# Kernel optimization log

Measured on AMD Instinct MI355X. Metric: run time of the kernel, lower is better.

The kernel has to match this reference:

```python
import jax, jax.numpy as jnp
import numpy as np

PATCH = 5
PAD = PATCH // 2
EPS = 0.01
NP2 = PATCH * PATCH  # 25 elements per patch


def _conv(x, w, b):
    # VALID conv, NCHW / OIHW
    y = jax.lax.conv_general_dilated(x, w, (1, 1), 'VALID',
                                     dimension_numbers=('NCHW', 'OIHW', 'NCHW'))
    return y + b[None, :, None, None]


def _maxpool2(x):
    return jax.lax.reduce_window(x, -jnp.inf, jax.lax.max,
                                 (1, 1, 2, 2), (1, 1, 2, 2), 'VALID')


def _normed_patches(x):
    # x: [B,C,H,W] -> zero-mean unit-std 5x5 patches [B,C,H,W,25]
    B, C, H, W = x.shape
    xp = jnp.pad(x, ((0, 0), (0, 0), (PAD, PAD), (PAD, PAD)))
    p = jnp.stack([xp[:, :, u:u + H, v:v + W]
                   for u in range(PATCH) for v in range(PATCH)], axis=-1)
    mu = p.mean(axis=-1, keepdims=True)
    sd = p.std(axis=-1, keepdims=True)
    return (p - mu) / (sd + EPS)


def _normxcorr(X, Y):
    # patch-wise NCC: each 5x5 patch of X at (i,j) vs patches of Y at rows
    # i-2..i+2 (zero outside) and ALL W columns -> [B, C*5*W, H, W]
    B, C, H, W = X.shape
    Xn = _normed_patches(X)            # [B,C,H,W,25]
    Yn = _normed_patches(Y)            # [B,C,H,W,25]
    Ynp = jnp.pad(Yn, ((0, 0), (0, 0), (PAD, PAD), (0, 0), (0, 0)))
    # row-shifted views: d=0..4 corresponds to displacement d-2
    Ysh = jnp.stack([Ynp[:, :, d:d + H] for d in range(PATCH)], axis=2)  # [B,C,5,H,W,25]
    out = jnp.einsum('bcijp,bcdikp->bcdkij', Xn, Ysh) / NP2  # [B,C,5,W,H,W]
    return out.reshape(B, C * PATCH * W, H, W)  # C*5*12 = 1500 channels


def _branch(x, w1, b1, w2, b2):
    x = _maxpool2(jax.nn.relu(_conv(x, w1, b1)))
    x = _maxpool2(jax.nn.relu(_conv(x, w2, b2)))
    return x  # [B,25,37,12]


def setup_inputs() -> dict:
    key = jax.random.key(0)
    ks = jax.random.split(key, 10)
    B = 64

    def n(k, shp, s=0.05):
        return jax.random.normal(k, shp, dtype=jnp.float32) * s

    return {
        'x1': jax.random.normal(ks[0], (B, 3, 160, 60), dtype=jnp.float32),
        'x2': jax.random.normal(ks[1], (B, 3, 160, 60), dtype=jnp.float32),
        'w_conv1': n(ks[2], (20, 3, 5, 5)), 'b_conv1': jnp.zeros((20,), jnp.float32),
        'w_conv2': n(ks[3], (25, 20, 5, 5)), 'b_conv2': jnp.zeros((25,), jnp.float32),
        'w_red1': n(ks[4], (25, 1500, 1, 1)), 'b_red1': jnp.zeros((25,), jnp.float32),
        'w_red2': n(ks[5], (25, 25, 3, 3)), 'b_red2': jnp.zeros((25,), jnp.float32),
        'w_lin1': n(ks[6], (500, 25 * 17 * 5)), 'b_lin1': jnp.zeros((500,), jnp.float32),
        'w_lin2': n(ks[7], (2, 500)), 'b_lin2': jnp.zeros((2,), jnp.float32),
    }


def reference(x1, x2, w_conv1, b_conv1, w_conv2, b_conv2,
              w_red1, b_red1, w_red2, b_red2,
              w_lin1, b_lin1, w_lin2, b_lin2):
    f1 = _branch(x1, w_conv1, b_conv1, w_conv2, b_conv2)  # [B,25,37,12]
    f2 = _branch(x2, w_conv1, b_conv1, w_conv2, b_conv2)
    r = jax.nn.relu(_normxcorr(f1, f2))                   # [B,1500,37,12]
    r = jax.nn.relu(_conv(r, w_red1, b_red1))             # [B,25,37,12]
    r = _maxpool2(_conv(r, w_red2, b_red2))               # [B,25,17,5]
    r = r.reshape(r.shape[0], -1)                         # [B,2125]
    r = r @ w_lin1.T + b_lin1
    r = r @ w_lin2.T + b_lin2
    return r
```

## Files before the change

### kernel.cpp

```cpp
#include <hip/hip_runtime.h>
#include <math.h>


static const long OFF_C1   = 0;
static const long OFF_F    = 5591040;
static const long OFF_MU   = 7011840;
static const long OFF_IV   = 8432640;
static const long OFF_WLT  = 9853440;
static const long OFF_PART = 0;
static const long OFF_RED1 = 3552000;
static const long OFF_R2P  = 4262400;
static const long OFF_WR1T = 4500000;
static const long OFF_LINP = 0;

__global__ __launch_bounds__(256) void k_wt(const float* __restrict__ wl1,
                                            float* __restrict__ wlt) {
  __shared__ float tile[32][33];
  int t0 = blockIdx.x * 32, o0 = blockIdx.y * 32;
  int lt = threadIdx.x % 32, lo = threadIdx.x / 32;
#pragma unroll
  for (int k = 0; k < 4; ++k) {
    int o = o0 + lo + 8 * k;
    if (o < 500 && t0 + lt < 2125)
      tile[lo + 8 * k][lt] = wl1[(long)o * 2125 + t0 + lt];
  }
  __syncthreads();
#pragma unroll
  for (int k = 0; k < 4; ++k) {
    int t = t0 + lo + 8 * k;
    if (t < 2125 && o0 + lt < 500)
      wlt[(long)t * 500 + o0 + lt] = tile[lt][lo + 8 * k];
  }
}

__global__ void k_wrt(const float* __restrict__ wr1, float* __restrict__ wr1t) {
  int idx = blockIdx.x * 256 + threadIdx.x;
  if (idx < 37500) {
    int o = idx / 1500, t = idx % 1500;
    wr1t[t * 28 + o] = wr1[idx];
  }
}

__global__ __launch_bounds__(128) void k_conv1(
    const float* __restrict__ x1, const float* __restrict__ x2,
    const float* __restrict__ w, const float* __restrict__ bias,
    float* __restrict__ out) {
  int img = blockIdx.x;
  int g   = blockIdx.y;
  int oc0 = blockIdx.z * 5;
  int p0  = g * 13;
  int R0  = 2 * p0;
  int tid = threadIdx.x;
  const float* x = (img < 64) ? (x1 + (long)img * 28800)
                              : (x2 + (long)(img - 64) * 28800);
  __shared__ float tile[3][30][60];

  for (int idx = tid; idx < 3 * 1800; idx += 128) {
    int ic = idx / 1800, rem = idx - ic * 1800;
    tile[ic][rem / 60][rem % 60] = x[ic * 9600 + R0 * 60 + rem];
  }
  __syncthreads();

  for (int item = tid; item < 364; item += 128) {
    int r = item / 28, j = item % 28;
    int lr = 2 * r, lc = 2 * j;
    float acc[5][4];
#pragma unroll
    for (int o = 0; o < 5; ++o) {
      acc[o][0] = 0.f; acc[o][1] = 0.f; acc[o][2] = 0.f; acc[o][3] = 0.f;
    }
#pragma unroll
    for (int ic = 0; ic < 3; ++ic) {
      float win[6][6];
#pragma unroll
      for (int u = 0; u < 6; ++u)
#pragma unroll
        for (int v = 0; v < 6; ++v) win[u][v] = tile[ic][lr + u][lc + v];
#pragma unroll
      for (int o = 0; o < 5; ++o) {
        const float* wq = w + ((oc0 + o) * 3 + ic) * 25;
#pragma unroll
        for (int u = 0; u < 5; ++u)
#pragma unroll
          for (int v = 0; v < 5; ++v) {
            float wv = wq[u * 5 + v];
            acc[o][0] = fmaf(wv, win[u][v], acc[o][0]);
            acc[o][1] = fmaf(wv, win[u][v + 1], acc[o][1]);
            acc[o][2] = fmaf(wv, win[u + 1][v], acc[o][2]);
            acc[o][3] = fmaf(wv, win[u + 1][v + 1], acc[o][3]);
          }
      }
    }
#pragma unroll
    for (int o = 0; o < 5; ++o) {
      float mx = fmaxf(fmaxf(acc[o][0], acc[o][1]), fmaxf(acc[o][2], acc[o][3]));
      out[((long)img * 20 + oc0 + o) * 2184 + (p0 + r) * 28 + j] =
          fmaxf(mx + bias[oc0 + o], 0.f);
    }
  }
}

__global__ __launch_bounds__(128) void k_conv2(
    const float* __restrict__ in, const float* __restrict__ w,
    const float* __restrict__ bias, float* __restrict__ out) {
  int img = blockIdx.x;
  int g   = blockIdx.y;
  int oc0 = blockIdx.z * 5;
  int p0  = g * 10;
  int ROWS = min(10, 37 - p0);
  int R0  = 2 * p0;
  int NR  = 2 * ROWS + 4;
  int tid = threadIdx.x;
  int r = tid / 12, j = tid % 12;
  bool active = (tid < 120) && (r < ROWS);
  const float* xin = in + (long)img * 43680;
  __shared__ float tile[2][24][29];

  {
    const float* src = xin + R0 * 28;
    for (int idx = tid; idx < NR * 28; idx += 128) {
      int row = idx / 28, col = idx - row * 28;
      tile[0][row][col] = src[idx];
    }
  }

  float acc[5][4];
#pragma unroll
  for (int o = 0; o < 5; ++o) {
    acc[o][0] = 0.f; acc[o][1] = 0.f; acc[o][2] = 0.f; acc[o][3] = 0.f;
  }
  int lr = 2 * r, lc = 2 * j;

  for (int ic = 0; ic < 20; ++ic) {
    __syncthreads();
    if (ic < 19) {
      const float* src = xin + (ic + 1) * 2184 + R0 * 28;
      int nxt = (ic + 1) & 1;
      for (int idx = tid; idx < NR * 28; idx += 128) {
        int row = idx / 28, col = idx - row * 28;
        tile[nxt][row][col] = src[idx];
      }
    }
    if (active) {
      int cur = ic & 1;
      float win[6][6];
#pragma unroll
      for (int u = 0; u < 6; ++u)
#pragma unroll
        for (int v = 0; v < 6; ++v) win[u][v] = tile[cur][lr + u][lc + v];
#pragma unroll
      for (int o = 0; o < 5; ++o) {
        const float* wq = w + ((oc0 + o) * 20 + ic) * 25;
#pragma unroll
        for (int u = 0; u < 5; ++u)
#pragma unroll
          for (int v = 0; v < 5; ++v) {
            float wv = wq[u * 5 + v];
            acc[o][0] = fmaf(wv, win[u][v], acc[o][0]);
            acc[o][1] = fmaf(wv, win[u][v + 1], acc[o][1]);
            acc[o][2] = fmaf(wv, win[u + 1][v], acc[o][2]);
            acc[o][3] = fmaf(wv, win[u + 1][v + 1], acc[o][3]);
          }
      }
    }
  }

  if (active) {
#pragma unroll
    for (int o = 0; o < 5; ++o) {
      float mx = fmaxf(fmaxf(acc[o][0], acc[o][1]), fmaxf(acc[o][2], acc[o][3]));
      out[((long)img * 25 + oc0 + o) * 444 + (p0 + r) * 12 + j] =
          fmaxf(mx + bias[oc0 + o], 0.f);
    }
  }
}

__global__ __launch_bounds__(448) void k_stats(
    const float* __restrict__ f, float* __restrict__ mu, float* __restrict__ iv) {
  int img = blockIdx.x, c = blockIdx.y;
  int t = threadIdx.x;
  if (t >= 444) return;
  int i = t / 12, j = t % 12;
  const float* fp = f + ((long)img * 25 + c) * 444;
  float s = 0.f, sq = 0.f;
#pragma unroll
  for (int u = 0; u < 5; ++u) {
    int gi = i + u - 2;
    if (gi < 0 || gi >= 37) continue;
#pragma unroll
    for (int v = 0; v < 5; ++v) {
      int gj = j + v - 2;
      if (gj < 0 || gj >= 12) continue;
      float vv = fp[gi * 12 + gj];
      s += vv;
      sq += vv * vv;
    }
  }
  float m = s * 0.04f;
  float var = sq * 0.04f - m * m;
  float sd = sqrtf(fmaxf(var, 0.f));
  long idx = ((long)img * 25 + c) * 444 + t;
  mu[idx] = m;
  iv[idx] = 1.f / (sd + 0.01f);
}

__global__ __launch_bounds__(128) void k_ncc(
    const float* __restrict__ f, const float* __restrict__ mu,
    const float* __restrict__ iv, const float* __restrict__ wr1t,
    float* __restrict__ part) {
  int b  = blockIdx.x;
  int g  = blockIdx.y;
  int cz = blockIdx.z;
  int i0 = g * 10;
  int ROWS = min(10, 37 - i0);
  int tid = threadIdx.x;
  int j = tid % 12, r = tid / 12;
  bool active = (r < ROWS);

  __shared__ float Xt[5][14][17];
  __shared__ __align__(16) float Yt[5][18][20];
  __shared__ float mX[5][10][12], iX[5][10][12];
  __shared__ float mY[5][14][12], iY[5][14][12];

  const float* Xf = f + (long)b * 25 * 444;
  const float* Yf = f + (long)(64 + b) * 25 * 444;
  const float* muX_g = mu + (long)b * 25 * 444;
  const float* ivX_g = iv + (long)b * 25 * 444;
  const float* muY_g = mu + (long)(64 + b) * 25 * 444;
  const float* ivY_g = iv + (long)(64 + b) * 25 * 444;

#pragma unroll 1
  for (int cc = 0; cc < 5; ++cc) {
    int c = cz * 5 + cc;
    for (int idx = tid; idx < 14 * 16; idx += 128) {
      int rr = idx >> 4, cl = idx & 15;
      int gi = i0 - 2 + rr, gj = cl - 2;
      Xt[cc][rr][cl] = (gi >= 0 && gi < 37 && gj >= 0 && gj < 12)
                           ? Xf[c * 444 + gi * 12 + gj] : 0.f;
    }
    for (int idx = tid; idx < 18 * 16; idx += 128) {
      int rr = idx >> 4, cl = idx & 15;
      int gi = i0 - 4 + rr, gj = cl - 2;
      Yt[cc][rr][cl] = (gi >= 0 && gi < 37 && gj >= 0 && gj < 12)
                           ? Yf[c * 444 + gi * 12 + gj] : 0.f;
    }
    for (int idx = tid; idx < 18 * 4; idx += 128) {
      int rr = idx >> 2;
      Yt[cc][rr][16 + (idx & 3)] = 0.f;
    }
    for (int idx = tid; idx < 120; idx += 128) {
      int rr = idx / 12, gj = idx % 12;
      int gi = i0 + rr;
      bool ok = gi < 37;
      mX[cc][rr][gj] = ok ? muX_g[c * 444 + gi * 12 + gj] : 0.f;
      iX[cc][rr][gj] = ok ? ivX_g[c * 444 + gi * 12 + gj] : 0.f;
    }
    for (int idx = tid; idx < 168; idx += 128) {
      int rr = idx / 12, gj = idx % 12;
      int gi = i0 - 2 + rr;
      bool ok = (gi >= 0 && gi < 37);
      float muv = ok ? muY_g[c * 444 + gi * 12 + gj] : 0.f;
      float ivv = ok ? ivY_g[c * 444 + gi * 12 + gj] : 0.f;
      mY[cc][rr][gj] = muv * ivv;
      iY[cc][rr][gj] = ivv;
    }
  }
  __syncthreads();

  float acc[25];
#pragma unroll
  for (int o = 0; o < 25; ++o) acc[o] = 0.f;

  if (active) {
#pragma unroll 1
    for (int cc = 0; cc < 5; ++cc) {
      int c = cz * 5 + cc;
      float xp[5][5];
#pragma unroll
      for (int u = 0; u < 5; ++u)
#pragma unroll
        for (int v = 0; v < 5; ++v) xp[u][v] = Xt[cc][r + u][j + v];
      float muXv = mX[cc][r][j], ivXv = iX[cc][r][j];
      float sX = ivXv * 0.04f;
      float tX = muXv * ivXv;
      const float* wb = wr1t + c * 1680;
#pragma unroll 1
      for (int d = 0; d < 5; ++d) {
        float rd[12];
#pragma unroll
        for (int k = 0; k < 12; ++k) rd[k] = 0.f;
#pragma unroll
        for (int u = 0; u < 5; ++u) {
          float yrow[16];
          const float* yb = &Yt[cc][r + d + u][0];
          *reinterpret_cast<float4*>(&yrow[0])  = *reinterpret_cast<const float4*>(yb);
          *reinterpret_cast<float4*>(&yrow[4])  = *reinterpret_cast<const float4*>(yb + 4);
          *reinterpret_cast<float4*>(&yrow[8])  = *reinterpret_cast<const float4*>(yb + 8);
          *reinterpret_cast<float4*>(&yrow[12]) = *reinterpret_cast<const float4*>(yb + 12);
#pragma unroll
          for (int k = 0; k < 12; ++k)
#pragma unroll
            for (int v = 0; v < 5; ++v)
              rd[k] = fmaf(xp[u][v], yrow[k + v], rd[k]);
        }
#pragma unroll
        for (int k = 0; k < 12; ++k) {
          float ivYv = iY[cc][r + d][k];
          float miYv = mY[cc][r + d][k];
          float rv = fmaxf(fmaf(-tX, miYv, rd[k] * sX * ivYv), 0.f);
          const float* wrow = wb + (d * 12 + k) * 28;
          float wv[25];
          *reinterpret_cast<float4*>(&wv[0])  = *reinterpret_cast<const float4*>(wrow);
          *reinterpret_cast<float4*>(&wv[4])  = *reinterpret_cast<const float4*>(wrow + 4);
          *reinterpret_cast<float4*>(&wv[8])  = *reinterpret_cast<const float4*>(wrow + 8);
          *reinterpret_cast<float4*>(&wv[12]) = *reinterpret_cast<const float4*>(wrow + 12);
          *reinterpret_cast<float4*>(&wv[16]) = *reinterpret_cast<const float4*>(wrow + 16);
          *reinterpret_cast<float4*>(&wv[20]) = *reinterpret_cast<const float4*>(wrow + 20);
          wv[24] = wrow[24];
#pragma unroll
          for (int o = 0; o < 25; ++o) acc[o] = fmaf(wv[o], rv, acc[o]);
        }
      }
    }
  }

  if (active) {
    int i = i0 + r;
    float* p = part + ((long)(b * 5 + cz) * 25) * 444 + i * 12 + j;
#pragma unroll
    for (int o = 0; o < 25; ++o) p[o * 444] = acc[o];
  }
}

__global__ __launch_bounds__(256) void k_red1sum(
    const float* __restrict__ part, const float* __restrict__ b1,
    float* __restrict__ red1) {
  int b = blockIdx.x;
  for (int item = threadIdx.x; item < 25 * 444; item += 256) {
    int o = item / 444, px = item % 444;
    float s = b1[o];
#pragma unroll
    for (int cz = 0; cz < 5; ++cz)
      s += part[((long)(b * 5 + cz) * 25 + o) * 444 + px];
    red1[((long)b * 25 + o) * 444 + px] = fmaxf(s, 0.f);
  }
}

__global__ __launch_bounds__(256) void k_red2(
    const float* __restrict__ red1, const float* __restrict__ w,
    const float* __restrict__ bias, float* __restrict__ r2p) {
  int b = blockIdx.x;
  int oc0 = blockIdx.y * 5;
  __shared__ float inb[25 * 444];
  __shared__ float wl[5 * 25 * 9];
  for (int idx = threadIdx.x; idx < 25 * 444; idx += 256)
    inb[idx] = red1[(long)b * 25 * 444 + idx];
  for (int idx = threadIdx.x; idx < 5 * 25 * 9; idx += 256)
    wl[idx] = w[oc0 * 25 * 9 + idx];
  __syncthreads();
  for (int item = threadIdx.x; item < 5 * 85; item += 256) {
    int ol = item / 85, rem = item % 85;
    int pi = rem / 5, pj = rem % 5;
    int ci0 = 2 * pi, cj0 = 2 * pj;
    float a00 = 0, a01 = 0, a10 = 0, a11 = 0;
    for (int ic = 0; ic < 25; ++ic) {
      const float* xp = inb + ic * 444 + ci0 * 12 + cj0;
      float win[4][4];
#pragma unroll
      for (int u = 0; u < 4; ++u)
#pragma unroll
        for (int v = 0; v < 4; ++v) win[u][v] = xp[u * 12 + v];
      const float* wq = wl + (ol * 25 + ic) * 9;
#pragma unroll
      for (int u = 0; u < 3; ++u)
#pragma unroll
        for (int v = 0; v < 3; ++v) {
          float wv = wq[u * 3 + v];
          a00 += wv * win[u][v];
          a01 += wv * win[u][v + 1];
          a10 += wv * win[u + 1][v];
          a11 += wv * win[u + 1][v + 1];
        }
    }
    float mx = fmaxf(fmaxf(a00, a01), fmaxf(a10, a11));
    r2p[(long)b * 2125 + (oc0 + ol) * 85 + rem] = mx + bias[oc0 + ol];
  }
}

__global__ __launch_bounds__(256) void k_lin1p(
    const float* __restrict__ r2p, const float* __restrict__ wlt,
    float* __restrict__ part) {
  int nb = blockIdx.x;
  int kc = blockIdx.y;
  int o0 = nb * 64, t0 = kc * 125;
  int tid = threadIdx.x;
  __shared__ float Xs[64][126];
  __shared__ float Ws[125][64];
  for (int idx = tid; idx < 64 * 125; idx += 256) {
    int b = idx / 125, tt = idx % 125;
    Xs[b][tt] = r2p[(long)b * 2125 + t0 + tt];
  }
  for (int idx = tid; idx < 125 * 64; idx += 256) {
    int tt = idx / 64, oo = idx % 64;
    int o = o0 + oo;
    Ws[tt][oo] = (o < 500) ? wlt[(long)(t0 + tt) * 500 + o] : 0.f;
  }
  __syncthreads();
  int b0 = (tid >> 4) << 2;
  int ol = (tid & 15) << 2;
  float acc[4][4];
#pragma unroll
  for (int i = 0; i < 4; ++i)
#pragma unroll
    for (int q = 0; q < 4; ++q) acc[i][q] = 0.f;
  for (int tt = 0; tt < 125; ++tt) {
    float xv[4];
#pragma unroll
    for (int i = 0; i < 4; ++i) xv[i] = Xs[b0 + i][tt];
    float4 wv = *reinterpret_cast<const float4*>(&Ws[tt][ol]);
#pragma unroll
    for (int i = 0; i < 4; ++i) {
      acc[i][0] += xv[i] * wv.x;
      acc[i][1] += xv[i] * wv.y;
      acc[i][2] += xv[i] * wv.z;
      acc[i][3] += xv[i] * wv.w;
    }
  }
#pragma unroll
  for (int i = 0; i < 4; ++i)
#pragma unroll
    for (int q = 0; q < 4; ++q)
      part[((long)kc * 64 + (b0 + i)) * 512 + o0 + ol + q] = acc[i][q];
}

__global__ __launch_bounds__(512) void k_lin2(
    const float* __restrict__ part, const float* __restrict__ bl1,
    const float* __restrict__ wl2, const float* __restrict__ bl2,
    float* __restrict__ out) {
  int b = blockIdx.x;
  int o = threadIdx.x;
  float s = 0.f;
  if (o < 500) {
#pragma unroll
    for (int kc = 0; kc < 17; ++kc) s += part[((long)kc * 64 + b) * 512 + o];
    s += bl1[o];
  }
  __shared__ float red0[512], red1s[512];
  red0[o]  = (o < 500) ? s * wl2[o] : 0.f;
  red1s[o] = (o < 500) ? s * wl2[500 + o] : 0.f;
  __syncthreads();
  for (int st = 256; st >= 1; st >>= 1) {
    if (o < st) { red0[o] += red0[o + st]; red1s[o] += red1s[o + st]; }
    __syncthreads();
  }
  if (o == 0) {
    out[b * 2 + 0] = red0[0] + bl2[0];
    out[b * 2 + 1] = red1s[0] + bl2[1];
  }
}

extern "C" void kernel_launch(void* const* d_in, const int* in_sizes, int n_in,
                              void* d_out, int out_size, void* d_ws, size_t ws_size,
                              hipStream_t stream) {
  const float* x1   = (const float*)d_in[0];
  const float* x2   = (const float*)d_in[1];
  const float* w1   = (const float*)d_in[2];
  const float* b1   = (const float*)d_in[3];
  const float* w2   = (const float*)d_in[4];
  const float* b2   = (const float*)d_in[5];
  const float* wr1  = (const float*)d_in[6];
  const float* br1  = (const float*)d_in[7];
  const float* wr2  = (const float*)d_in[8];
  const float* br2  = (const float*)d_in[9];
  const float* wl1  = (const float*)d_in[10];
  const float* bl1  = (const float*)d_in[11];
  const float* wl2  = (const float*)d_in[12];
  const float* bl2  = (const float*)d_in[13];
  float* out = (float*)d_out;
  float* ws  = (float*)d_ws;

  float* c1    = ws + OFF_C1;
  float* f     = ws + OFF_F;
  float* mu    = ws + OFF_MU;
  float* iv    = ws + OFF_IV;
  float* wlt   = ws + OFF_WLT;
  float* part  = ws + OFF_PART;
  float* red1  = ws + OFF_RED1;
  float* r2p   = ws + OFF_R2P;
  float* wr1t  = ws + OFF_WR1T;
  float* linp  = ws + OFF_LINP;

  hipLaunchKernelGGL(k_wt, dim3(67, 16), dim3(256), 0, stream, wl1, wlt);

  hipLaunchKernelGGL(k_conv1, dim3(128, 6, 4), dim3(128), 0, stream, x1, x2, w1, b1, c1);
  hipLaunchKernelGGL(k_conv2, dim3(128, 4, 5), dim3(128), 0, stream, c1, w2, b2, f);

  hipLaunchKernelGGL(k_wrt, dim3(147), dim3(256), 0, stream, wr1, wr1t);

  hipLaunchKernelGGL(k_stats, dim3(128, 25), dim3(448), 0, stream, f, mu, iv);
  hipLaunchKernelGGL(k_ncc, dim3(64, 4, 5), dim3(128), 0, stream, f, mu, iv, wr1t, part);
  hipLaunchKernelGGL(k_red1sum, dim3(64), dim3(256), 0, stream, part, br1, red1);
  hipLaunchKernelGGL(k_red2, dim3(64, 5), dim3(256), 0, stream, red1, wr2, br2, r2p);

  hipLaunchKernelGGL(k_lin1p, dim3(8, 17), dim3(256), 0, stream, r2p, wlt, linp);
  hipLaunchKernelGGL(k_lin2, dim3(64), dim3(512), 0, stream, linp, bl1, wl2, bl2, out);
}
```

Baseline: 355.9 us.

## Split NCC across all channels with atomic reduction, fold bias/relu into red2

The NCC kernel now launches one block per channel (25 in z) instead of five channel groups, giving a wider grid. Partial results are accumulated directly into red1 with atomicAdd after a memset, which removes the separate k_red1sum kernel and the partial buffer. The bias add and ReLU move into k_red2's load path. conv1 also gets a restructured shared-memory tile load and float2 window reads. The change adds heavy atomic traffic (25 adds per output element), makes float summation order nondeterministic, and introduces an extra memset.

Result: faster. 335.0 us (-5.9%).

```diff
diff --git a/kernel.cpp b/kernel.cpp
--- a/kernel.cpp
+++ b/kernel.cpp
@@ -7,7 +7,6 @@
 static const long OFF_MU   = 7011840;
 static const long OFF_IV   = 8432640;
 static const long OFF_WLT  = 9853440;
-static const long OFF_PART = 0;
 static const long OFF_RED1 = 3552000;
 static const long OFF_R2P  = 4262400;
 static const long OFF_WR1T = 4500000;
@@ -53,11 +52,21 @@
   int tid = threadIdx.x;
   const float* x = (img < 64) ? (x1 + (long)img * 28800)
                               : (x2 + (long)(img - 64) * 28800);
-  __shared__ float tile[3][30][60];
-
-  for (int idx = tid; idx < 3 * 1800; idx += 128) {
-    int ic = idx / 1800, rem = idx - ic * 1800;
-    tile[ic][rem / 60][rem % 60] = x[ic * 9600 + R0 * 60 + rem];
+  __shared__ __align__(16) float tile[3][30][60];
+
+  {
+    int col = tid % 60, row0 = tid / 60;
+    if (tid < 120) {
+#pragma unroll
+      for (int ic = 0; ic < 3; ++ic) {
+        const float* s = x + ic * 9600 + R0 * 60 + col;
+        float* d = &tile[ic][0][col];
+#pragma unroll
+        for (int row = 0; row < 15; ++row) {
+          d[(row0 + 2 * row) * 60] = s[(row0 + 2 * row) * 60];
+        }
+      }
+    }
   }
   __syncthreads();
 
@@ -73,9 +82,14 @@
     for (int ic = 0; ic < 3; ++ic) {
       float win[6][6];
 #pragma unroll
-      for (int u = 0; u < 6; ++u)
-#pragma unroll
-        for (int v = 0; v < 6; ++v) win[u][v] = tile[ic][lr + u][lc + v];
+      for (int u = 0; u < 6; ++u) {
+        const float* rp = &tile[ic][lr + u][lc];
+        float2 a = *reinterpret_cast<const float2*>(rp);
+        float2 b = *reinterpret_cast<const float2*>(rp + 2);
+        float2 c = *reinterpret_cast<const float2*>(rp + 4);
+        win[u][0] = a.x; win[u][1] = a.y; win[u][2] = b.x;
+        win[u][3] = b.y; win[u][4] = c.x; win[u][5] = c.y;
+      }
 #pragma unroll
       for (int o = 0; o < 5; ++o) {
         const float* wq = w + ((oc0 + o) * 3 + ic) * 25;
@@ -207,154 +221,133 @@
 __global__ __launch_bounds__(128) void k_ncc(
     const float* __restrict__ f, const float* __restrict__ mu,
     const float* __restrict__ iv, const float* __restrict__ wr1t,
-    float* __restrict__ part) {
+    float* __restrict__ red1) {
   int b  = blockIdx.x;
   int g  = blockIdx.y;
-  int cz = blockIdx.z;
+  int c  = blockIdx.z;
   int i0 = g * 10;
   int ROWS = min(10, 37 - i0);
   int tid = threadIdx.x;
   int j = tid % 12, r = tid / 12;
   bool active = (r < ROWS);
 
-  __shared__ float Xt[5][14][17];
-  __shared__ __align__(16) float Yt[5][18][20];
-  __shared__ float mX[5][10][12], iX[5][10][12];
-  __shared__ float mY[5][14][12], iY[5][14][12];
-
-  const float* Xf = f + (long)b * 25 * 444;
-  const float* Yf = f + (long)(64 + b) * 25 * 444;
-  const float* muX_g = mu + (long)b * 25 * 444;
-  const float* ivX_g = iv + (long)b * 25 * 444;
-  const float* muY_g = mu + (long)(64 + b) * 25 * 444;
-  const float* ivY_g = iv + (long)(64 + b) * 25 * 444;
-
+  __shared__ float Xt[14][17];
+  __shared__ __align__(16) float Yt[18][20];
+  __shared__ float mX[10][12], iX[10][12];
+  __shared__ float mY[14][12], iY[14][12];
+
+  const float* Xf = f + (long)b * 25 * 444 + c * 444;
+  const float* Yf = f + (long)(64 + b) * 25 * 444 + c * 444;
+  const float* muX_g = mu + (long)b * 25 * 444 + c * 444;
+  const float* ivX_g = iv + (long)b * 25 * 444 + c * 444;
+  const float* muY_g = mu + (long)(64 + b) * 25 * 444 + c * 444;
+  const float* ivY_g = iv + (long)(64 + b) * 25 * 444 + c * 444;
+
+  for (int idx = tid; idx < 14 * 16; idx += 128) {
+    int rr = idx >> 4, cl = idx & 15;
+    int gi = i0 - 2 + rr, gj = cl - 2;
+    Xt[rr][cl] = (gi >= 0 && gi < 37 && gj >= 0 && gj < 12)
+                     ? Xf[gi * 12 + gj] : 0.f;
+  }
+  for (int idx = tid; idx < 18 * 16; idx += 128) {
+    int rr = idx >> 4, cl = idx & 15;
+    int gi = i0 - 4 + rr, gj = cl - 2;
+    Yt[rr][cl] = (gi >= 0 && gi < 37 && gj >= 0 && gj < 12)
+                     ? Yf[gi * 12 + gj] : 0.f;
+  }
+  for (int idx = tid; idx < 18 * 4; idx += 128) {
+    int rr = idx >> 2;
+    Yt[rr][16 + (idx & 3)] = 0.f;
+  }
+  for (int idx = tid; idx < 120; idx += 128) {
+    int rr = idx / 12, gj = idx % 12;
+    int gi = i0 + rr;
+    bool ok = gi < 37;
+    mX[rr][gj] = ok ? muX_g[gi * 12 + gj] : 0.f;
+    iX[rr][gj] = ok ? ivX_g[gi * 12 + gj] : 0.f;
+  }
+  for (int idx = tid; idx < 168; idx += 128) {
+    int rr = idx / 12, gj = idx % 12;
+    int gi = i0 - 2 + rr;
+    bool ok = (gi >= 0 && gi < 37);
+    float muv = ok ? muY_g[gi * 12 + gj] : 0.f;
+    float ivv = ok ? ivY_g[gi * 12 + gj] : 0.f;
+    mY[rr][gj] = muv * ivv;
+    iY[rr][gj] = ivv;
+  }
+  __syncthreads();
+
+  float acc[25];
+#pragma unroll
+  for (int o = 0; o < 25; ++o) acc[o] = 0.f;
+
+  if (active) {
+    float xp[5][5];
+#pragma unroll
+    for (int u = 0; u < 5; ++u)
+#pragma unroll
+      for (int v = 0; v < 5; ++v) xp[u][v] = Xt[r + u][j + v];
+    float muXv = mX[r][j], ivXv = iX[r][j];
+    float sX = ivXv * 0.04f;
+    float tX = muXv * ivXv;
+    const float* wb = wr1t + c * 1680;
 #pragma unroll 1
-  for (int cc = 0; cc < 5; ++cc) {
-    int c = cz * 5 + cc;
-    for (int idx = tid; idx < 14 * 16; idx += 128) {
-      int rr = idx >> 4, cl = idx & 15;
-      int gi = i0 - 2 + rr, gj = cl - 2;
-      Xt[cc][rr][cl] = (gi >= 0 && gi < 37 && gj >= 0 && gj < 12)
-                           ? Xf[c * 444 + gi * 12 + gj] : 0.f;
-    }
-    for (int idx = tid; idx < 18 * 16; idx += 128) {
-      int rr = idx >> 4, cl = idx & 15;
-      int gi = i0 - 4 + rr, gj = cl - 2;
-      Yt[cc][rr][cl] = (gi >= 0 && gi < 37 && gj >= 0 && gj < 12)
-                           ? Yf[c * 444 + gi * 12 + gj] : 0.f;
-    }
-    for (int idx = tid; idx < 18 * 4; idx += 128) {
-      int rr = idx >> 2;
-      Yt[cc][rr][16 + (idx & 3)] = 0.f;
-    }
-    for (int idx = tid; idx < 120; idx += 128) {
-      int rr = idx / 12, gj = idx % 12;
-      int gi = i0 + rr;
-      bool ok = gi < 37;
-      mX[cc][rr][gj] = ok ? muX_g[c * 444 + gi * 12 + gj] : 0.f;
-      iX[cc][rr][gj] = ok ? ivX_g[c * 444 + gi * 12 + gj] : 0.f;
-    }
-    for (int idx = tid; idx < 168; idx += 128) {
-      int rr = idx / 12, gj = idx % 12;
-      int gi = i0 - 2 + rr;
-      bool ok = (gi >= 0 && gi < 37);
-      float muv = ok ? muY_g[c * 444 + gi * 12 + gj] : 0.f;
-      float ivv = ok ? ivY_g[c * 444 + gi * 12 + gj] : 0.f;
-      mY[cc][rr][gj] = muv * ivv;
-      iY[cc][rr][gj] = ivv;
-    }
-  }
-  __syncthreads();
-
-  float acc[25];
-#pragma unroll
-  for (int o = 0; o < 25; ++o) acc[o] = 0.f;
-
-  if (active) {
-#pragma unroll 1
-    for (int cc = 0; cc < 5; ++cc) {
-      int c = cz * 5 + cc;
-      float xp[5][5];
-#pragma unroll
-      for (int u = 0; u < 5; ++u)
-#pragma unroll
-        for (int v = 0; v < 5; ++v) xp[u][v] = Xt[cc][r + u][j + v];
-      float muXv = mX[cc][r][j], ivXv = iX[cc][r][j];
-      float sX = ivXv * 0.04f;
-      float tX = muXv * ivXv;
-      const float* wb = wr1t + c * 1680;
-#pragma unroll 1
-      for (int d = 0; d < 5; ++d) {
-        float rd[12];
-#pragma unroll
-        for (int k = 0; k < 12; ++k) rd[k] = 0.f;
-#pragma unroll
-        for (int u = 0; u < 5; ++u) {
-          float yrow[16];
-          const float* yb = &Yt[cc][r + d + u][0];
-          *reinterpret_cast<float4*>(&yrow[0])  = *reinterpret_cast<const float4*>(yb);
-          *reinterpret_cast<float4*>(&yrow[4])  = *reinterpret_cast<const float4*>(yb + 4);
-          *reinterpret_cast<float4*>(&yrow[8])  = *reinterpret_cast<const float4*>(yb + 8);
-          *reinterpret_cast<float4*>(&yrow[12]) = *reinterpret_cast<const float4*>(yb + 12);
-#pragma unroll
-          for (int k = 0; k < 12; ++k)
-#pragma unroll
-            for (int v = 0; v < 5; ++v)
-              rd[k] = fmaf(xp[u][v], yrow[k + v], rd[k]);
-        }
-#pragma unroll
-        for (int k = 0; k < 12; ++k) {
-          float ivYv = iY[cc][r + d][k];
-          float miYv = mY[cc][r + d][k];
-          float rv = fmaxf(fmaf(-tX, miYv, rd[k] * sX * ivYv), 0.f);
-          const float* wrow = wb + (d * 12 + k) * 28;
-          float wv[25];
-          *reinterpret_cast<float4*>(&wv[0])  = *reinterpret_cast<const float4*>(wrow);
-          *reinterpret_cast<float4*>(&wv[4])  = *reinterpret_cast<const float4*>(wrow + 4);
-          *reinterpret_cast<float4*>(&wv[8])  = *reinterpret_cast<const float4*>(wrow + 8);
-          *reinterpret_cast<float4*>(&wv[12]) = *reinterpret_cast<const float4*>(wrow + 12);
-          *reinterpret_cast<float4*>(&wv[16]) = *reinterpret_cast<const float4*>(wrow + 16);
-          *reinterpret_cast<float4*>(&wv[20]) = *reinterpret_cast<const float4*>(wrow + 20);
-          wv[24] = wrow[24];
-#pragma unroll
-          for (int o = 0; o < 25; ++o) acc[o] = fmaf(wv[o], rv, acc[o]);
-        }
+    for (int d = 0; d < 5; ++d) {
+      float rd[12];
+#pragma unroll
+      for (int k = 0; k < 12; ++k) rd[k] = 0.f;
+#pragma unroll
+      for (int u = 0; u < 5; ++u) {
+        float yrow[16];
+        const float* yb = &Yt[r + d + u][0];
+        *reinterpret_cast<float4*>(&yrow[0])  = *reinterpret_cast<const float4*>(yb);
+        *reinterpret_cast<float4*>(&yrow[4])  = *reinterpret_cast<const float4*>(yb + 4);
+        *reinterpret_cast<float4*>(&yrow[8])  = *reinterpret_cast<const float4*>(yb + 8);
+        *reinterpret_cast<float4*>(&yrow[12]) = *reinterpret_cast<const float4*>(yb + 12);
+#pragma unroll
+        for (int k = 0; k < 12; ++k)
+#pragma unroll
+          for (int v = 0; v < 5; ++v)
+            rd[k] = fmaf(xp[u][v], yrow[k + v], rd[k]);
+      }
+#pragma unroll
+      for (int k = 0; k < 12; ++k) {
+        float ivYv = iY[r + d][k];
+        float miYv = mY[r + d][k];
+        float rv = fmaxf(fmaf(-tX, miYv, rd[k] * sX * ivYv), 0.f);
+        const float* wrow = wb + (d * 12 + k) * 28;
+        float wv[25];
+        *reinterpret_cast<float4*>(&wv[0])  = *reinterpret_cast<const float4*>(wrow);
+        *reinterpret_cast<float4*>(&wv[4])  = *reinterpret_cast<const float4*>(wrow + 4);
+        *reinterpret_cast<float4*>(&wv[8])  = *reinterpret_cast<const float4*>(wrow + 8);
+        *reinterpret_cast<float4*>(&wv[12]) = *reinterpret_cast<const float4*>(wrow + 12);
+        *reinterpret_cast<float4*>(&wv[16]) = *reinterpret_cast<const float4*>(wrow + 16);
+        *reinterpret_cast<float4*>(&wv[20]) = *reinterpret_cast<const float4*>(wrow + 20);
+        wv[24] = wrow[24];
+#pragma unroll
+        for (int o = 0; o < 25; ++o) acc[o] = fmaf(wv[o], rv, acc[o]);
       }
     }
   }
 
   if (active) {
     int i = i0 + r;
-    float* p = part + ((long)(b * 5 + cz) * 25) * 444 + i * 12 + j;
-#pragma unroll
-    for (int o = 0; o < 25; ++o) p[o * 444] = acc[o];
-  }
-}
-
-__global__ __launch_bounds__(256) void k_red1sum(
-    const float* __restrict__ part, const float* __restrict__ b1,
-    float* __restrict__ red1) {
-  int b = blockIdx.x;
-  for (int item = threadIdx.x; item < 25 * 444; item += 256) {
-    int o = item / 444, px = item % 444;
-    float s = b1[o];
-#pragma unroll
-    for (int cz = 0; cz < 5; ++cz)
-      s += part[((long)(b * 5 + cz) * 25 + o) * 444 + px];
-    red1[((long)b * 25 + o) * 444 + px] = fmaxf(s, 0.f);
+    float* p = red1 + (long)b * 25 * 444 + i * 12 + j;
+#pragma unroll
+    for (int o = 0; o < 25; ++o) atomicAdd(p + o * 444, acc[o]);
   }
 }
 
 __global__ __launch_bounds__(256) void k_red2(
-    const float* __restrict__ red1, const float* __restrict__ w,
-    const float* __restrict__ bias, float* __restrict__ r2p) {
+    const float* __restrict__ red1, const float* __restrict__ br1,
+    const float* __restrict__ w, const float* __restrict__ bias,
+    float* __restrict__ r2p) {
   int b = blockIdx.x;
   int oc0 = blockIdx.y * 5;
   __shared__ float inb[25 * 444];
   __shared__ float wl[5 * 25 * 9];
   for (int idx = threadIdx.x; idx < 25 * 444; idx += 256)
-    inb[idx] = red1[(long)b * 25 * 444 + idx];
+    inb[idx] = fmaxf(red1[(long)b * 25 * 444 + idx] + br1[idx / 444], 0.f);
   for (int idx = threadIdx.x; idx < 5 * 25 * 9; idx += 256)
     wl[idx] = w[oc0 * 25 * 9 + idx];
   __syncthreads();
@@ -484,7 +477,6 @@
   float* mu    = ws + OFF_MU;
   float* iv    = ws + OFF_IV;
   float* wlt   = ws + OFF_WLT;
-  float* part  = ws + OFF_PART;
   float* red1  = ws + OFF_RED1;
   float* r2p   = ws + OFF_R2P;
   float* wr1t  = ws + OFF_WR1T;
@@ -498,9 +490,11 @@
   hipLaunchKernelGGL(k_wrt, dim3(147), dim3(256), 0, stream, wr1, wr1t);
 
   hipLaunchKernelGGL(k_stats, dim3(128, 25), dim3(448), 0, stream, f, mu, iv);
-  hipLaunchKernelGGL(k_ncc, dim3(64, 4, 5), dim3(128), 0, stream, f, mu, iv, wr1t, part);
-  hipLaunchKernelGGL(k_red1sum, dim3(64), dim3(256), 0, stream, part, br1, red1);
-  hipLaunchKernelGGL(k_red2, dim3(64, 5), dim3(256), 0, stream, red1, wr2, br2, r2p);
+
+  hipMemsetAsync(red1, 0, 710400 * sizeof(float), stream);
+  hipLaunchKernelGGL(k_ncc, dim3(64, 4, 25), dim3(128), 0, stream, f, mu, iv, wr1t, red1);
+
+  hipLaunchKernelGGL(k_red2, dim3(64, 5), dim3(256), 0, stream, red1, br1, wr2, br2, r2p);
 
   hipLaunchKernelGGL(k_lin1p, dim3(8, 17), dim3(256), 0, stream, r2p, wlt, linp);
   hipLaunchKernelGGL(k_lin2, dim3(64), dim3(512), 0, stream, linp, bl1, wl2, bl2, out);
```
